# Performance work log

Measured on AMD Instinct MI355X. Metric: run time of the kernel, lower is better.

The kernel has to match this reference:

```python
import jax, jax.numpy as jnp
import numpy as np

IN_DIM = 256
OUT_DIM = 256

def setup_inputs() -> dict:
    key = jax.random.key(0)
    k1, k2, k3, k4 = jax.random.split(key, 4)
    B, N, K, D = 4, 10000, 16, IN_DIM
    x = jax.random.normal(k1, (B, N, D), dtype=jnp.float32)
    neigh = jax.random.randint(k2, (N, K), 0, N, dtype=jnp.int64)
    # nn.Linear(2*in_dim, out_dim): W [out, 2*in], b [out]
    bound = 1.0 / np.sqrt(2 * D)
    W = jax.random.uniform(k3, (OUT_DIM, 2 * D), minval=-bound, maxval=bound, dtype=jnp.float32)
    b = jax.random.uniform(k4, (OUT_DIM,), minval=-bound, maxval=bound, dtype=jnp.float32)
    return {"x": x, "neigh": neigh, "W": W, "b": b}

def reference(x, neigh, W, b):
    # x: [B,N,D], neigh: [N,K] with -1 = padding
    mask = (neigh >= 0)                                # [N,K]
    idx = jnp.clip(neigh, 0, None)                     # [N,K]
    # batch_gather_nodes: x_nei[b,n,k,:] = x[b, idx[n,k], :]
    x_nei = x[:, idx, :]                               # [B,N,K,D]
    x_nei = x_nei * mask[None, :, :, None].astype(x.dtype)
    denom = jnp.clip(mask.sum(axis=1), 1, None).astype(x.dtype)  # [N]
    agg = x_nei.sum(axis=2) / denom[None, :, None]     # [B,N,D]
    h = jnp.concatenate([x, agg], axis=-1)             # [B,N,2D]
    return jax.nn.relu(jnp.einsum('bnd,od->bno', h, W) + b)
```

## Files before the change

### kernel.cpp

```cpp
#include <hip/hip_runtime.h>
#include <hip/hip_bf16.h>
#include <stdint.h>

#define B_   4
#define N_   10000
#define K_   16
#define D_   256
#define OUT_ 256
#define KDIM 512
#define M_   (B_ * N_)
#define CW   32
#define NCH  8
#define CHUNK_ELEMS ((size_t)N_ * B_ * CW)

typedef __attribute__((ext_vector_type(8))) short          short8;
typedef __attribute__((ext_vector_type(8))) unsigned short ushort8;
typedef __attribute__((ext_vector_type(4))) float          f32x4;
typedef __attribute__((ext_vector_type(4))) unsigned short ushort4_t;

__device__ inline unsigned short f2bf(float f) {
    __hip_bfloat16 h = __float2bfloat16(f);
    return *reinterpret_cast<unsigned short*>(&h);
}
__device__ inline float bf2f(unsigned short u) {
    unsigned int v = ((unsigned int)u) << 16;
    return __builtin_bit_cast(float, v);
}

__global__ __launch_bounds__(256) void prep(const float* __restrict__ x,
                                            const float* __restrict__ W,
                                            unsigned short* __restrict__ xc,
                                            unsigned short* __restrict__ Wb) {
    const int t = threadIdx.x;
    if (blockIdx.x < 5000) {
        const int n  = blockIdx.x * 2 + (t >> 7);
        const int b  = (t >> 5) & 3;
        const int c0 = (t & 31) * 8;
        const float4* xr = (const float4*)(x + ((size_t)b * N_ + n) * D_ + c0);
        float4 v0 = xr[0];
        float4 v1 = xr[1];
        ushort8 s;
        s[0] = f2bf(v0.x); s[1] = f2bf(v0.y); s[2] = f2bf(v0.z); s[3] = f2bf(v0.w);
        s[4] = f2bf(v1.x); s[5] = f2bf(v1.y); s[6] = f2bf(v1.z); s[7] = f2bf(v1.w);
        const int ch  = c0 >> 5;
        const int col = c0 & 31;
        *(ushort8*)(xc + (size_t)ch * CHUNK_ELEMS + ((size_t)n * B_ + b) * CW + col) = s;
    } else {
        int g = (blockIdx.x - 5000) * 256 + t;
        float4 v = ((const float4*)W)[g];
        ushort4_t s;
        s.x = f2bf(v.x); s.y = f2bf(v.y); s.z = f2bf(v.z); s.w = f2bf(v.w);
        ((ushort4_t*)Wb)[g] = s;
    }
}

__global__ __launch_bounds__(256) void gather_agg2(const unsigned short* __restrict__ xc,
                                                   const int*            __restrict__ neigh,
                                                   unsigned short*       __restrict__ hagg) {
    const int c   = blockIdx.x & 7;
    const int g   = blockIdx.x >> 3;
    const int n0  = g * 16;
    const int tid = threadIdx.x;

    __shared__ int   idx_s[16 * K_];
    __shared__ float inv_s[16];

    idx_s[tid] = neigh[n0 * K_ + tid];
    __syncthreads();
    if (tid < 16) {
        int cnt = 0;
#pragma unroll
        for (int k = 0; k < K_; ++k) cnt += idx_s[tid * K_ + k] >= 0 ? 1 : 0;
        inv_s[tid] = 1.0f / (float)(cnt > 1 ? cnt : 1);
    }
    __syncthreads();

    const int q  = tid & 3;
    const int tl = tid >> 2;
    const int ns = tl >> 2;
    const int b  = tl & 3;

    const unsigned short* xcc = xc + (size_t)c * CHUNK_ELEMS;

    int jj[K_];
#pragma unroll
    for (int k = 0; k < K_; ++k) jj[k] = idx_s[ns * K_ + k];

    ushort8 vv[K_];
#pragma unroll
    for (int k = 0; k < K_; ++k) {
        const int jc = jj[k] >= 0 ? jj[k] : 0;
        vv[k] = *(const ushort8*)(xcc + ((size_t)jc * B_ + b) * CW + q * 8);
    }

    float acc[8] = {0.f, 0.f, 0.f, 0.f, 0.f, 0.f, 0.f, 0.f};
#pragma unroll
    for (int k = 0; k < K_; ++k) {
        const float m = jj[k] >= 0 ? 1.f : 0.f;
#pragma unroll
        for (int e = 0; e < 8; ++e) acc[e] += bf2f(vv[k][e]) * m;
    }
    const float inv = inv_s[ns];

    ushort8 s;
#pragma unroll
    for (int e = 0; e < 8; ++e) s[e] = f2bf(acc[e] * inv);
    *(ushort8*)(hagg + ((size_t)b * N_ + n0 + ns) * D_ + c * CW + q * 8) = s;
}

__global__ __launch_bounds__(256) void gemm_bt3(const unsigned short* __restrict__ xc,
                                                const unsigned short* __restrict__ hagg,
                                                const unsigned short* __restrict__ Bm,
                                                const float* __restrict__ bias,
                                                float* __restrict__ out) {
    __shared__ unsigned short As[64 * 32];
    __shared__ unsigned short Bs[256 * 32];

    const int tid    = threadIdx.x;
    const int w      = tid >> 6;
    const int lane   = tid & 63;
    const int tile_m = blockIdx.x * 64;
    const int q      = lane >> 4;
    const int r16    = lane & 15;

    const int crow = lane >> 2;
    const int kofs = (lane & 3) * 8;

    const unsigned short* ps[4];
    const unsigned short* pa[4];
#pragma unroll
    for (int c = 0; c < 4; ++c) {
        const int m  = tile_m + c * 16 + crow;
        const int b  = (m >= N_) + (m >= 2 * N_) + (m >= 3 * N_);
        const int n  = m - b * N_;
        ps[c] = xc + ((size_t)n * B_ + b) * CW + kofs;
        pa[c] = hagg + (size_t)m * D_ + kofs;
    }

    f32x4 acc[4][4] = {};

    for (int kk = 0; kk < KDIM; kk += 32) {
        const int kidx = kk >> 5;
#pragma unroll
        for (int t = 0; t < 5; ++t) {
            const int c = w * 5 + t;
            if (c < 4) {
                const unsigned short* ga = (kk < D_)
                    ? ps[c] + (size_t)kidx * CHUNK_ELEMS
                    : pa[c] + (kk - D_);
                __builtin_amdgcn_global_load_lds(
                    (const __attribute__((address_space(1))) void*)ga,
                    (__attribute__((address_space(3))) void*)(As + c * 512),
                    16, 0, 0);
            } else {
                const int row = (c - 4) * 16 + crow;
                const unsigned short* gb = Bm + (size_t)row * KDIM + kk + kofs;
                __builtin_amdgcn_global_load_lds(
                    (const __attribute__((address_space(1))) void*)gb,
                    (__attribute__((address_space(3))) void*)(Bs + (c - 4) * 512),
                    16, 0, 0);
            }
        }
        __syncthreads();

        short8 a[4], bf[4];
#pragma unroll
        for (int i = 0; i < 4; ++i)
            a[i] = *(const short8*)(As + (i * 16 + r16) * 32 + q * 8);
#pragma unroll
        for (int j = 0; j < 4; ++j)
            bf[j] = *(const short8*)(Bs + (w * 64 + j * 16 + r16) * 32 + q * 8);

#pragma unroll
        for (int i = 0; i < 4; ++i)
#pragma unroll
            for (int j = 0; j < 4; ++j)
                acc[i][j] = __builtin_amdgcn_mfma_f32_16x16x32_bf16(a[i], bf[j], acc[i][j], 0, 0, 0);

        __syncthreads();
    }

    float bj[4];
#pragma unroll
    for (int j = 0; j < 4; ++j)
        bj[j] = bias[w * 64 + j * 16 + r16];

#pragma unroll
    for (int i = 0; i < 4; ++i) {
#pragma unroll
        for (int reg = 0; reg < 4; ++reg) {
            const int m = tile_m + i * 16 + q * 4 + reg;
            float* orow = out + (size_t)m * OUT_ + w * 64;
#pragma unroll
            for (int j = 0; j < 4; ++j) {
                float v = acc[i][j][reg] + bj[j];
                orow[j * 16 + r16] = v > 0.f ? v : 0.f;
            }
        }
    }
}

extern "C" void kernel_launch(void* const* d_in, const int* in_sizes, int n_in,
                              void* d_out, int out_size, void* d_ws, size_t ws_size,
                              hipStream_t stream) {
    const float* x     = (const float*)d_in[0];
    const int*   neigh = (const int*)d_in[1];
    const float* W     = (const float*)d_in[2];
    const float* bias  = (const float*)d_in[3];
    float*       out   = (float*)d_out;

    unsigned short* Wb   = (unsigned short*)d_ws;
    unsigned short* xc   = Wb + OUT_ * KDIM;
    unsigned short* hagg = xc + NCH * CHUNK_ELEMS;

    prep<<<5000 + 128, 256, 0, stream>>>(x, W, xc, Wb);
    gather_agg2<<<(N_ / 16) * NCH, 256, 0, stream>>>(xc, neigh, hagg);
    gemm_bt3<<<M_ / 64, 256, 0, stream>>>(xc, hagg, Wb, bias, out);
}
```

Before: 132.4 us.

## Apply linear layer before neighbor aggregation, then gather projected features

Uses linearity to reorder the work: x is first multiplied by both halves of W (self and neighbor weights) in one GEMM over K=256. The self half goes to an fp32 buffer and the neighbor half to a chunked bf16 buffer. A gather kernel then averages the projected neighbor rows and adds the self term and bias, then applies ReLU. This drops the separate x-to-bf16 prep pass and the hagg intermediate, and halves the GEMM reduction depth, but it writes and re-reads an extra fp32 M×256 intermediate.

Result: slower. 144.3 us (+9.0%).

```diff
diff --git a/kernel.cpp b/kernel.cpp
--- a/kernel.cpp
+++ b/kernel.cpp
@@ -7,7 +7,6 @@
 #define K_   16
 #define D_   256
 #define OUT_ 256
-#define KDIM 512
 #define M_   (B_ * N_)
 #define CW   32
 #define NCH  8
@@ -27,36 +26,121 @@
     return __builtin_bit_cast(float, v);
 }
 
-__global__ __launch_bounds__(256) void prep(const float* __restrict__ x,
-                                            const float* __restrict__ W,
-                                            unsigned short* __restrict__ xc,
-                                            unsigned short* __restrict__ Wb) {
-    const int t = threadIdx.x;
-    if (blockIdx.x < 5000) {
-        const int n  = blockIdx.x * 2 + (t >> 7);
-        const int b  = (t >> 5) & 3;
-        const int c0 = (t & 31) * 8;
-        const float4* xr = (const float4*)(x + ((size_t)b * N_ + n) * D_ + c0);
-        float4 v0 = xr[0];
-        float4 v1 = xr[1];
+__global__ __launch_bounds__(256) void wprep(const float* __restrict__ W,
+                                             unsigned short* __restrict__ Wb) {
+    const int g  = blockIdx.x * 256 + threadIdx.x;
+    const int op = g >> 6;
+    const int k0 = (g & 63) * 4;
+    const float* src = (op < OUT_) ? (W + (size_t)op * 512 + k0)
+                                   : (W + (size_t)(op - OUT_) * 512 + 256 + k0);
+    const float4 v = *(const float4*)src;
+    ushort4_t s;
+    s.x = f2bf(v.x); s.y = f2bf(v.y); s.z = f2bf(v.z); s.w = f2bf(v.w);
+    *(ushort4_t*)(Wb + (size_t)op * 256 + k0) = s;
+}
+
+__global__ __launch_bounds__(256) void gemm_fused(const float* __restrict__ x,
+                                                  const unsigned short* __restrict__ Wb,
+                                                  float* __restrict__ y1,
+                                                  unsigned short* __restrict__ y2c) {
+    __shared__ unsigned short As[64 * 32];
+    __shared__ unsigned short Bs[256 * 32];
+
+    const int tid    = threadIdx.x;
+    const int w      = tid >> 6;
+    const int lane   = tid & 63;
+    const int q      = lane >> 4;
+    const int r16    = lane & 15;
+    const int half   = blockIdx.x & 1;
+    const int tile_m = (blockIdx.x >> 1) * 64;
+
+    const int crow = lane >> 2;
+    const int kofs = (lane & 3) * 8;
+
+    const int arow  = tid >> 2;
+    const int acol8 = (tid & 3) * 8;
+    const float* xrow = x + (size_t)(tile_m + arow) * D_ + acol8;
+
+    const unsigned short* bsrc =
+        Wb + ((size_t)(half * OUT_ + w * 64 + crow)) * D_ + kofs;
+
+    f32x4 acc[4][4] = {};
+
+    float4 va0 = *(const float4*)(xrow);
+    float4 va1 = *(const float4*)(xrow + 4);
+
+    for (int kk = 0; kk < D_; kk += 32) {
+#pragma unroll
+        for (int t = 0; t < 4; ++t) {
+            __builtin_amdgcn_global_load_lds(
+                (const __attribute__((address_space(1))) void*)(bsrc + (size_t)t * 16 * D_ + kk),
+                (__attribute__((address_space(3))) void*)(Bs + (w * 4 + t) * 512),
+                16, 0, 0);
+        }
         ushort8 s;
-        s[0] = f2bf(v0.x); s[1] = f2bf(v0.y); s[2] = f2bf(v0.z); s[3] = f2bf(v0.w);
-        s[4] = f2bf(v1.x); s[5] = f2bf(v1.y); s[6] = f2bf(v1.z); s[7] = f2bf(v1.w);
-        const int ch  = c0 >> 5;
-        const int col = c0 & 31;
-        *(ushort8*)(xc + (size_t)ch * CHUNK_ELEMS + ((size_t)n * B_ + b) * CW + col) = s;
+        s[0] = f2bf(va0.x); s[1] = f2bf(va0.y); s[2] = f2bf(va0.z); s[3] = f2bf(va0.w);
+        s[4] = f2bf(va1.x); s[5] = f2bf(va1.y); s[6] = f2bf(va1.z); s[7] = f2bf(va1.w);
+        *(ushort8*)(As + arow * 32 + acol8) = s;
+        if (kk + 32 < D_) {
+            va0 = *(const float4*)(xrow + kk + 32);
+            va1 = *(const float4*)(xrow + kk + 36);
+        }
+        __syncthreads();
+
+        short8 a[4], bf[4];
+#pragma unroll
+        for (int i = 0; i < 4; ++i)
+            a[i] = *(const short8*)(As + (i * 16 + r16) * 32 + q * 8);
+#pragma unroll
+        for (int j = 0; j < 4; ++j)
+            bf[j] = *(const short8*)(Bs + (w * 64 + j * 16 + r16) * 32 + q * 8);
+
+#pragma unroll
+        for (int i = 0; i < 4; ++i)
+#pragma unroll
+            for (int j = 0; j < 4; ++j)
+                acc[i][j] = __builtin_amdgcn_mfma_f32_16x16x32_bf16(a[i], bf[j], acc[i][j], 0, 0, 0);
+
+        __syncthreads();
+    }
+
+    if (half == 0) {
+#pragma unroll
+        for (int i = 0; i < 4; ++i) {
+#pragma unroll
+            for (int reg = 0; reg < 4; ++reg) {
+                const int m = tile_m + i * 16 + q * 4 + reg;
+                float* row = y1 + (size_t)m * OUT_ + w * 64;
+#pragma unroll
+                for (int j = 0; j < 4; ++j)
+                    row[j * 16 + r16] = acc[i][j][reg];
+            }
+        }
     } else {
-        int g = (blockIdx.x - 5000) * 256 + t;
-        float4 v = ((const float4*)W)[g];
-        ushort4_t s;
-        s.x = f2bf(v.x); s.y = f2bf(v.y); s.z = f2bf(v.z); s.w = f2bf(v.w);
-        ((ushort4_t*)Wb)[g] = s;
-    }
-}
-
-__global__ __launch_bounds__(256) void gather_agg2(const unsigned short* __restrict__ xc,
-                                                   const int*            __restrict__ neigh,
-                                                   unsigned short*       __restrict__ hagg) {
+#pragma unroll
+        for (int i = 0; i < 4; ++i) {
+#pragma unroll
+            for (int reg = 0; reg < 4; ++reg) {
+                const int m = tile_m + i * 16 + q * 4 + reg;
+                const int b = (m >= N_) + (m >= 2 * N_) + (m >= 3 * N_);
+                const int n = m - b * N_;
+                unsigned short* rbase = y2c + (size_t)(n * B_ + b) * CW;
+#pragma unroll
+                for (int j = 0; j < 4; ++j) {
+                    const int o2 = w * 64 + j * 16 + r16;
+                    rbase[(size_t)(o2 >> 5) * CHUNK_ELEMS + (o2 & 31)] =
+                        f2bf(acc[i][j][reg]);
+                }
+            }
+        }
+    }
+}
+
+__global__ __launch_bounds__(256) void gather_out(const unsigned short* __restrict__ y2c,
+                                                  const float* __restrict__ y1,
+                                                  const int*   __restrict__ neigh,
+                                                  const float* __restrict__ bias,
+                                                  float* __restrict__ out) {
     const int c   = blockIdx.x & 7;
     const int g   = blockIdx.x >> 3;
     const int n0  = g * 16;
@@ -80,7 +164,7 @@
     const int ns = tl >> 2;
     const int b  = tl & 3;
 
-    const unsigned short* xcc = xc + (size_t)c * CHUNK_ELEMS;
+    const unsigned short* ycc = y2c + (size_t)c * CHUNK_ELEMS;
 
     int jj[K_];
 #pragma unroll
@@ -90,8 +174,14 @@
 #pragma unroll
     for (int k = 0; k < K_; ++k) {
         const int jc = jj[k] >= 0 ? jj[k] : 0;
-        vv[k] = *(const ushort8*)(xcc + ((size_t)jc * B_ + b) * CW + q * 8);
-    }
+        vv[k] = *(const ushort8*)(ycc + ((size_t)jc * B_ + b) * CW + q * 8);
+    }
+
+    const size_t mo = (size_t)(b * N_ + n0 + ns) * OUT_ + c * CW + q * 8;
+    const f32x4 s0 = *(const f32x4*)(y1 + mo);
+    const f32x4 s1 = *(const f32x4*)(y1 + mo + 4);
+    const f32x4 b0 = *(const f32x4*)(bias + c * CW + q * 8);
+    const f32x4 b1 = *(const f32x4*)(bias + c * CW + q * 8 + 4);
 
     float acc[8] = {0.f, 0.f, 0.f, 0.f, 0.f, 0.f, 0.f, 0.f};
 #pragma unroll
@@ -102,102 +192,16 @@
     }
     const float inv = inv_s[ns];
 
-    ushort8 s;
-#pragma unroll
-    for (int e = 0; e < 8; ++e) s[e] = f2bf(acc[e] * inv);
-    *(ushort8*)(hagg + ((size_t)b * N_ + n0 + ns) * D_ + c * CW + q * 8) = s;
-}
-
-__global__ __launch_bounds__(256) void gemm_bt3(const unsigned short* __restrict__ xc,
-                                                const unsigned short* __restrict__ hagg,
-                                                const unsigned short* __restrict__ Bm,
-                                                const float* __restrict__ bias,
-                                                float* __restrict__ out) {
-    __shared__ unsigned short As[64 * 32];
-    __shared__ unsigned short Bs[256 * 32];
-
-    const int tid    = threadIdx.x;
-    const int w      = tid >> 6;
-    const int lane   = tid & 63;
-    const int tile_m = blockIdx.x * 64;
-    const int q      = lane >> 4;
-    const int r16    = lane & 15;
-
-    const int crow = lane >> 2;
-    const int kofs = (lane & 3) * 8;
-
-    const unsigned short* ps[4];
-    const unsigned short* pa[4];
-#pragma unroll
-    for (int c = 0; c < 4; ++c) {
-        const int m  = tile_m + c * 16 + crow;
-        const int b  = (m >= N_) + (m >= 2 * N_) + (m >= 3 * N_);
-        const int n  = m - b * N_;
-        ps[c] = xc + ((size_t)n * B_ + b) * CW + kofs;
-        pa[c] = hagg + (size_t)m * D_ + kofs;
-    }
-
-    f32x4 acc[4][4] = {};
-
-    for (int kk = 0; kk < KDIM; kk += 32) {
-        const int kidx = kk >> 5;
-#pragma unroll
-        for (int t = 0; t < 5; ++t) {
-            const int c = w * 5 + t;
-            if (c < 4) {
-                const unsigned short* ga = (kk < D_)
-                    ? ps[c] + (size_t)kidx * CHUNK_ELEMS
-                    : pa[c] + (kk - D_);
-                __builtin_amdgcn_global_load_lds(
-                    (const __attribute__((address_space(1))) void*)ga,
-                    (__attribute__((address_space(3))) void*)(As + c * 512),
-                    16, 0, 0);
-            } else {
-                const int row = (c - 4) * 16 + crow;
-                const unsigned short* gb = Bm + (size_t)row * KDIM + kk + kofs;
-                __builtin_amdgcn_global_load_lds(
-                    (const __attribute__((address_space(1))) void*)gb,
-                    (__attribute__((address_space(3))) void*)(Bs + (c - 4) * 512),
-                    16, 0, 0);
-            }
-        }
-        __syncthreads();
-
-        short8 a[4], bf[4];
-#pragma unroll
-        for (int i = 0; i < 4; ++i)
-            a[i] = *(const short8*)(As + (i * 16 + r16) * 32 + q * 8);
-#pragma unroll
-        for (int j = 0; j < 4; ++j)
-            bf[j] = *(const short8*)(Bs + (w * 64 + j * 16 + r16) * 32 + q * 8);
-
-#pragma unroll
-        for (int i = 0; i < 4; ++i)
-#pragma unroll
-            for (int j = 0; j < 4; ++j)
-                acc[i][j] = __builtin_amdgcn_mfma_f32_16x16x32_bf16(a[i], bf[j], acc[i][j], 0, 0, 0);
-
-        __syncthreads();
-    }
-
-    float bj[4];
-#pragma unroll
-    for (int j = 0; j < 4; ++j)
-        bj[j] = bias[w * 64 + j * 16 + r16];
-
-#pragma unroll
-    for (int i = 0; i < 4; ++i) {
-#pragma unroll
-        for (int reg = 0; reg < 4; ++reg) {
-            const int m = tile_m + i * 16 + q * 4 + reg;
-            float* orow = out + (size_t)m * OUT_ + w * 64;
-#pragma unroll
-            for (int j = 0; j < 4; ++j) {
-                float v = acc[i][j][reg] + bj[j];
-                orow[j * 16 + r16] = v > 0.f ? v : 0.f;
-            }
-        }
-    }
+    f32x4 o0, o1;
+#pragma unroll
+    for (int e = 0; e < 4; ++e) {
+        float v0 = acc[e] * inv + s0[e] + b0[e];
+        float v1 = acc[e + 4] * inv + s1[e] + b1[e];
+        o0[e] = v0 > 0.f ? v0 : 0.f;
+        o1[e] = v1 > 0.f ? v1 : 0.f;
+    }
+    __builtin_nontemporal_store(o0, (f32x4*)(out + mo));
+    __builtin_nontemporal_store(o1, (f32x4*)(out + mo + 4));
 }
 
 extern "C" void kernel_launch(void* const* d_in, const int* in_sizes, int n_in,
@@ -209,11 +213,11 @@
     const float* bias  = (const float*)d_in[3];
     float*       out   = (float*)d_out;
 
-    unsigned short* Wb   = (unsigned short*)d_ws;
-    unsigned short* xc   = Wb + OUT_ * KDIM;
-    unsigned short* hagg = xc + NCH * CHUNK_ELEMS;
-
-    prep<<<5000 + 128, 256, 0, stream>>>(x, W, xc, Wb);
-    gather_agg2<<<(N_ / 16) * NCH, 256, 0, stream>>>(xc, neigh, hagg);
-    gemm_bt3<<<M_ / 64, 256, 0, stream>>>(xc, hagg, Wb, bias, out);
-}
+    unsigned short* Wb  = (unsigned short*)d_ws;
+    float*          y1  = (float*)(Wb + 512 * D_);
+    unsigned short* y2c = (unsigned short*)(y1 + (size_t)M_ * OUT_);
+
+    wprep<<<128, 256, 0, stream>>>(W, Wb);
+    gemm_fused<<<(M_ / 64) * 2, 256, 0, stream>>>(x, Wb, y1, y2c);
+    gather_out<<<(N_ / 16) * NCH, 256, 0, stream>>>(y2c, y1, neigh, bias, out);
+}
```
